# Performance work log

Hardware: AMD Instinct MI355X
Metric: run time of the kernel (lower is better)

The kernel has to match this reference:

```python
import jax, jax.numpy as jnp
import numpy as np

N = 120000
G = 64  # voxel grid side
HID = 128
INP = 320
CIN = HID + INP  # 448
K = 27


def _build_neighbor_map(rng):
    # unique occupied voxel cells
    cells = rng.choice(G ** 3, size=N, replace=False)
    xs = cells // (G * G)
    ys = (cells // G) % G
    zs = cells % G
    order = np.argsort(cells)
    sk = cells[order]
    offs = np.array([(dx, dy, dz) for dx in (-1, 0, 1) for dy in (-1, 0, 1) for dz in (-1, 0, 1)], dtype=np.int64)
    nx = xs[:, None] + offs[None, :, 0]
    ny = ys[:, None] + offs[None, :, 1]
    nz = zs[:, None] + offs[None, :, 2]
    valid = (nx >= 0) & (nx < G) & (ny >= 0) & (ny < G) & (nz >= 0) & (nz < G)
    nkey = (nx * G + ny) * G + nz
    pos = np.clip(np.searchsorted(sk, nkey), 0, N - 1)
    found = valid & (sk[pos] == nkey)
    return np.where(found, order[pos], -1).astype(np.int32)  # (N, 27)


def setup_inputs() -> dict:
    key = jax.random.key(0)
    ks = jax.random.split(key, 12)
    rng = np.random.default_rng(0)
    nbr = jnp.asarray(_build_neighbor_map(rng))
    s_conv = 1.0 / np.sqrt(K * CIN)
    s_lin = 1.0 / np.sqrt(CIN)
    return {
        "h": jax.random.normal(ks[0], (N, HID), jnp.float32),
        "x": jax.random.normal(ks[1], (N, INP), jnp.float32),
        "nbr": nbr,
        "Wz": jax.random.normal(ks[2], (K, CIN, HID), jnp.float32) * s_conv,
        "Wz_pt": jax.random.normal(ks[3], (CIN, HID), jnp.float32) * s_lin,
        "bz": jnp.zeros((HID,), jnp.float32),
        "Wr": jax.random.normal(ks[4], (K, CIN, HID), jnp.float32) * s_conv,
        "Wr_pt": jax.random.normal(ks[5], (CIN, HID), jnp.float32) * s_lin,
        "br": jnp.zeros((HID,), jnp.float32),
        "Wq": jax.random.normal(ks[6], (K, CIN, HID), jnp.float32) * s_conv,
        "Wq_pt": jax.random.normal(ks[7], (CIN, HID), jnp.float32) * s_lin,
        "bq": jnp.zeros((HID,), jnp.float32),
    }


def _sconv3d(F, nbr, W, W_pt, b_pt):
    # sparse 3x3x3 conv (gather + matmul accumulate over 27 offsets, no conv bias)
    # followed by voxel_to_point (identity here) + point_transforms linear.
    mask = (nbr >= 0)
    idx = jnp.where(mask, nbr, 0)
    out = F @ W_pt + b_pt  # point transform branch
    for k in range(K):  # fixed small kernel-offset loop
        g = F[idx[:, k]] * mask[:, k:k + 1].astype(F.dtype)  # (N, CIN)
        out = out + g @ W[k]
    return out


def reference(h, x, nbr, Wz, Wz_pt, bz, Wr, Wr_pt, br, Wq, Wq_pt, bq):
    hx = jnp.concatenate([h, x], axis=1)  # (N, 448)
    z = jax.nn.sigmoid(_sconv3d(hx, nbr, Wz, Wz_pt, bz))
    r = jax.nn.sigmoid(_sconv3d(hx, nbr, Wr, Wr_pt, br))
    rx = jnp.concatenate([r * h, x], axis=1)
    q = jnp.tanh(_sconv3d(rx, nbr, Wq, Wq_pt, bq))
    return (1.0 - z) * h + z * q
```

## Files before the change

kernel.cpp:

```cpp
#include <hip/hip_runtime.h>

#define NPTS   120000
#define NOFF   28
#define CHUNKS 7

typedef __bf16 bf16;
typedef __bf16 bf16x8 __attribute__((ext_vector_type(8)));
typedef float  f32x4  __attribute__((ext_vector_type(4)));

__global__ void wprep1(const float* __restrict__ Wz, const float* __restrict__ Wzp,
                       const float* __restrict__ Wr, const float* __restrict__ Wrp,
                       bf16* __restrict__ WB1)
{
    int bid  = blockIdx.x;
    int koff = bid / 56;
    int rem  = bid % 56;
    int ch   = rem / 8;
    int kseg = rem % 8;
    int n    = threadIdx.x;
    int cinb = ch * 64 + kseg * 8;
    bf16x8 v;
    if (n < 128) {
        int col = n;
        #pragma unroll
        for (int j = 0; j < 8; ++j) {
            int cin = cinb + j;
            float w = (koff < 27) ? Wz[((long)koff * 448 + cin) * 128 + col]
                                  : Wzp[(long)cin * 128 + col];
            v[j] = (bf16)w;
        }
    } else {
        int col = n - 128;
        #pragma unroll
        for (int j = 0; j < 8; ++j) {
            int cin = cinb + j;
            float w = (koff < 27) ? Wr[((long)koff * 448 + cin) * 128 + col]
                                  : Wrp[(long)cin * 128 + col];
            v[j] = (bf16)w;
        }
    }
    *(bf16x8*)(WB1 + ((long)bid * 256 + n) * 8) = v;
}

__global__ void wprep2(const float* __restrict__ Wq, const float* __restrict__ Wqp,
                       bf16* __restrict__ WB2)
{
    int bid  = blockIdx.x;
    int koff = bid / 56;
    int rem  = bid % 56;
    int ch   = rem / 8;
    int kseg = rem % 8;
    int n    = threadIdx.x;
    int cinb = ch * 64 + kseg * 8;
    bf16x8 v;
    #pragma unroll
    for (int j = 0; j < 8; ++j) {
        int cin = cinb + j;
        float w = (koff < 27) ? Wq[((long)koff * 448 + cin) * 128 + n]
                              : Wqp[(long)cin * 128 + n];
        v[j] = (bf16)w;
    }
    *(bf16x8*)(WB2 + ((long)bid * 128 + n) * 8) = v;
}

__global__ void fprep(const float* __restrict__ h, const float* __restrict__ x,
                      bf16* __restrict__ F1)
{
    long g = (long)blockIdx.x * blockDim.x + threadIdx.x;
    if (g >= (long)NPTS * 56) return;
    int p = (int)(g / 56);
    int c = (int)(g % 56) * 8;
    const float* src = (c < 128) ? h + (long)p * 128 + c
                                 : x + (long)p * 320 + (c - 128);
    float4 a = ((const float4*)src)[0];
    float4 b = ((const float4*)src)[1];
    bf16x8 v;
    v[0] = (bf16)a.x; v[1] = (bf16)a.y; v[2] = (bf16)a.z; v[3] = (bf16)a.w;
    v[4] = (bf16)b.x; v[5] = (bf16)b.y; v[6] = (bf16)b.z; v[7] = (bf16)b.w;
    *(bf16x8*)(F1 + (long)p * 448 + c) = v;
}

template<int MROWS, int NCOLS, int GATE>
__global__ __launch_bounds__(512)
void gconv(const bf16* __restrict__ F, const int* __restrict__ nbr,
           const bf16* __restrict__ WB, const float* __restrict__ b0,
           const float* __restrict__ b1, const float* __restrict__ hbuf,
           float* __restrict__ zbuf, bf16* __restrict__ f2,
           float* __restrict__ out, const bf16* __restrict__ zrow)
{
    constexpr int THREADS = 512;
    constexpr int MW = MROWS / 64;
    constexpr int AP = 8 * MROWS / THREADS;
    constexpr int BP = 8 * NCOLS / THREADS;

    __shared__ __align__(16) bf16 lA[8 * MROWS * 8];
    __shared__ __align__(16) bf16 lB[8 * NCOLS * 8];
    __shared__ int lidx[MROWS];

    const int t    = threadIdx.x;
    const int lane = t & 63;
    const int w    = t >> 6;
    const int m0   = (w % MW) * 64;
    const int n0   = (w / MW) * 64;
    const int base = blockIdx.x * MROWS;
    const int ar   = t % MROWS;
    const int aks0 = t / MROWS;

    f32x4 acc[4][4];
    #pragma unroll
    for (int i = 0; i < 4; ++i)
        #pragma unroll
        for (int j = 0; j < 4; ++j)
            acc[i][j] = {0.f, 0.f, 0.f, 0.f};

    const bf16x8* lAv = (const bf16x8*)lA;
    const bf16x8* lBv = (const bf16x8*)lB;

    for (int koff = 0; koff < NOFF; ++koff) {
        __syncthreads();
        if (t < MROWS) {
            int p = base + t;
            int idx = -1;
            if (p < NPTS) idx = (koff == 27) ? p : nbr[(long)p * 27 + koff];
            lidx[t] = idx;
        }
        __syncthreads();
        const int myidx = lidx[ar];
        const bf16* row1 = (myidx >= 0) ? (F + (long)myidx * 448) : zrow;
        const bf16* row2 = row1;
        if constexpr (GATE == 2)
            row2 = (myidx >= 0) ? (f2 + (long)myidx * 128) : zrow;

        for (int ch = 0; ch < CHUNKS; ++ch) {
            const bf16* asrc = (GATE == 2 && ch < 2) ? (row2 + ch * 64)
                                                     : (row1 + ch * 64);
            #pragma unroll
            for (int p = 0; p < AP; ++p) {
                int kseg = aks0 + p * (THREADS / MROWS);
                __builtin_amdgcn_global_load_lds(
                    (void*)(asrc + kseg * 8),
                    (void*)(lA + ((long)t + (long)p * THREADS) * 8),
                    16, 0, 0);
            }
            const bf16* bsrc = WB + (long)(koff * CHUNKS + ch) * (NCOLS * 64);
            #pragma unroll
            for (int p = 0; p < BP; ++p) {
                __builtin_amdgcn_global_load_lds(
                    (void*)(bsrc + ((long)t + (long)p * THREADS) * 8),
                    (void*)(lB + ((long)t + (long)p * THREADS) * 8),
                    16, 0, 0);
            }
            __syncthreads();
            #pragma unroll
            for (int kk = 0; kk < 2; ++kk) {
                const int aseg = kk * 4 + (lane >> 4);
                bf16x8 af[4], bfr[4];
                #pragma unroll
                for (int mi = 0; mi < 4; ++mi)
                    af[mi] = lAv[aseg * MROWS + m0 + mi * 16 + (lane & 15)];
                #pragma unroll
                for (int ni = 0; ni < 4; ++ni)
                    bfr[ni] = lBv[aseg * NCOLS + n0 + ni * 16 + (lane & 15)];
                #pragma unroll
                for (int mi = 0; mi < 4; ++mi)
                    #pragma unroll
                    for (int ni = 0; ni < 4; ++ni)
                        acc[mi][ni] = __builtin_amdgcn_mfma_f32_16x16x32_bf16(
                            af[mi], bfr[ni], acc[mi][ni], 0, 0, 0);
            }
            __syncthreads();
        }
    }

    const int quad = lane >> 4;
    const int lc   = lane & 15;
    #pragma unroll
    for (int mi = 0; mi < 4; ++mi) {
        int rb = m0 + mi * 16 + quad * 4;
        #pragma unroll
        for (int ni = 0; ni < 4; ++ni) {
            int c = n0 + ni * 16 + lc;
            f32x4 v = acc[mi][ni];
            #pragma unroll
            for (int rg = 0; rg < 4; ++rg) {
                int p = base + rb + rg;
                if (p < NPTS) {
                    float pre = v[rg];
                    if constexpr (GATE == 1) {
                        if (c < 128) {
                            float z = 1.f / (1.f + __expf(-(pre + b0[c])));
                            zbuf[(long)p * 128 + c] = z;
                        } else {
                            int cc = c - 128;
                            float r = 1.f / (1.f + __expf(-(pre + b1[cc])));
                            f2[(long)p * 128 + cc] = (bf16)(r * hbuf[(long)p * 128 + cc]);
                        }
                    } else {
                        float q  = tanhf(pre + b0[c]);
                        float z  = zbuf[(long)p * 128 + c];
                        float hv = hbuf[(long)p * 128 + c];
                        out[(long)p * 128 + c] = (1.f - z) * hv + z * q;
                    }
                }
            }
        }
    }
}

extern "C" void kernel_launch(void* const* d_in, const int* in_sizes, int n_in,
                              void* d_out, int out_size, void* d_ws, size_t ws_size,
                              hipStream_t stream)
{
    const float* h   = (const float*)d_in[0];
    const float* x   = (const float*)d_in[1];
    const int*   nbr = (const int*)d_in[2];
    const float* Wz  = (const float*)d_in[3];
    const float* Wzp = (const float*)d_in[4];
    const float* bz  = (const float*)d_in[5];
    const float* Wr  = (const float*)d_in[6];
    const float* Wrp = (const float*)d_in[7];
    const float* br  = (const float*)d_in[8];
    const float* Wq  = (const float*)d_in[9];
    const float* Wqp = (const float*)d_in[10];
    const float* bq  = (const float*)d_in[11];
    float* out = (float*)d_out;

    char* ws = (char*)d_ws;
    bf16* WB1 = (bf16*)ws;  ws += (size_t)1568 * 256 * 8 * 2;
    bf16* WB2 = (bf16*)ws;  ws += (size_t)1568 * 128 * 8 * 2;
    bf16* F1  = (bf16*)ws;  ws += (size_t)NPTS * 448 * 2;
    bf16* F2  = (bf16*)ws;  ws += (size_t)NPTS * 128 * 2;
    bf16* zrow = (bf16*)ws; ws += 1024;
    float* zbuf = out;

    hipMemsetAsync(zrow, 0, 1024, stream);
    wprep1<<<1568, 256, 0, stream>>>(Wz, Wzp, Wr, Wrp, WB1);
    wprep2<<<1568, 128, 0, stream>>>(Wq, Wqp, WB2);
    long groups = (long)NPTS * 56;
    fprep<<<(int)((groups + 255) / 256), 256, 0, stream>>>(h, x, F1);

    gconv<128, 256, 1><<<(NPTS + 127) / 128, 512, 0, stream>>>(
        F1, nbr, WB1, bz, br, h, zbuf, F2, nullptr, zrow);
    gconv<256, 128, 2><<<(NPTS + 255) / 256, 512, 0, stream>>>(
        F1, nbr, WB2, bq, nullptr, h, zbuf, F2, out, zrow);
}
```

Before: 1.537 ms.

## Multi-stage LDS pipeline for gather-conv with prefetched neighbor indices

Replaces the single-buffered load/sync/compute loop with a 2- or 3-stage circular LDS buffer. The next gathered rows and weight chunks are issued asynchronously while MFMAs run on the current stage, using explicit vmcnt waits and raw barriers. All 28 offset indices for the block are preloaded into LDS up front, which removes the two per-offset barriers, and setprio raises priority around the MFMA burst. The extra stages increase LDS use and may reduce occupancy.

```diff
diff --git a/kernel.cpp b/kernel.cpp
--- a/kernel.cpp
+++ b/kernel.cpp
@@ -3,6 +3,7 @@
 #define NPTS   120000
 #define NOFF   28
 #define CHUNKS 7
+#define NSTEP  (NOFF * CHUNKS)
 
 typedef __bf16 bf16;
 typedef __bf16 bf16x8 __attribute__((ext_vector_type(8)));
@@ -89,13 +90,17 @@
            float* __restrict__ out, const bf16* __restrict__ zrow)
 {
     constexpr int THREADS = 512;
-    constexpr int MW = MROWS / 64;
-    constexpr int AP = 8 * MROWS / THREADS;
-    constexpr int BP = 8 * NCOLS / THREADS;
-
-    __shared__ __align__(16) bf16 lA[8 * MROWS * 8];
-    __shared__ __align__(16) bf16 lB[8 * NCOLS * 8];
-    __shared__ int lidx[MROWS];
+    constexpr int MW  = MROWS / 64;
+    constexpr int AP  = 8 * MROWS / THREADS;
+    constexpr int BP  = 8 * NCOLS / THREADS;
+    constexpr int STG = (GATE == 1) ? 3 : 2;
+    constexpr int ASZ = 8 * MROWS * 8;
+    constexpr int BSZ = 8 * NCOLS * 8;
+    constexpr int LPB = AP + BP;
+
+    __shared__ __align__(16) bf16 lA[STG * ASZ];
+    __shared__ __align__(16) bf16 lB[STG * BSZ];
+    __shared__ int lidx[NOFF * MROWS];
 
     const int t    = threadIdx.x;
     const int lane = t & 63;
@@ -106,6 +111,15 @@
     const int ar   = t % MROWS;
     const int aks0 = t / MROWS;
 
+    for (int i = t; i < NOFF * MROWS; i += THREADS) {
+        int k = i / MROWS, r = i - k * MROWS;
+        int p = base + r;
+        int idx = -1;
+        if (p < NPTS) idx = (k == 27) ? p : nbr[(long)p * 27 + k];
+        lidx[i] = idx;
+    }
+    __syncthreads();
+
     f32x4 acc[4][4];
     #pragma unroll
     for (int i = 0; i < 4; ++i)
@@ -113,63 +127,77 @@
         for (int j = 0; j < 4; ++j)
             acc[i][j] = {0.f, 0.f, 0.f, 0.f};
 
-    const bf16x8* lAv = (const bf16x8*)lA;
-    const bf16x8* lBv = (const bf16x8*)lB;
-
-    for (int koff = 0; koff < NOFF; ++koff) {
-        __syncthreads();
-        if (t < MROWS) {
-            int p = base + t;
-            int idx = -1;
-            if (p < NPTS) idx = (koff == 27) ? p : nbr[(long)p * 27 + koff];
-            lidx[t] = idx;
-        }
-        __syncthreads();
-        const int myidx = lidx[ar];
-        const bf16* row1 = (myidx >= 0) ? (F + (long)myidx * 448) : zrow;
-        const bf16* row2 = row1;
-        if constexpr (GATE == 2)
-            row2 = (myidx >= 0) ? (f2 + (long)myidx * 128) : zrow;
-
-        for (int ch = 0; ch < CHUNKS; ++ch) {
-            const bf16* asrc = (GATE == 2 && ch < 2) ? (row2 + ch * 64)
-                                                     : (row1 + ch * 64);
-            #pragma unroll
-            for (int p = 0; p < AP; ++p) {
-                int kseg = aks0 + p * (THREADS / MROWS);
-                __builtin_amdgcn_global_load_lds(
-                    (void*)(asrc + kseg * 8),
-                    (void*)(lA + ((long)t + (long)p * THREADS) * 8),
-                    16, 0, 0);
-            }
-            const bf16* bsrc = WB + (long)(koff * CHUNKS + ch) * (NCOLS * 64);
-            #pragma unroll
-            for (int p = 0; p < BP; ++p) {
-                __builtin_amdgcn_global_load_lds(
-                    (void*)(bsrc + ((long)t + (long)p * THREADS) * 8),
-                    (void*)(lB + ((long)t + (long)p * THREADS) * 8),
-                    16, 0, 0);
-            }
-            __syncthreads();
-            #pragma unroll
-            for (int kk = 0; kk < 2; ++kk) {
-                const int aseg = kk * 4 + (lane >> 4);
-                bf16x8 af[4], bfr[4];
-                #pragma unroll
-                for (int mi = 0; mi < 4; ++mi)
-                    af[mi] = lAv[aseg * MROWS + m0 + mi * 16 + (lane & 15)];
+    auto stage = [&](int s) {
+        const int koff = s / CHUNKS;
+        const int ch   = s - koff * CHUNKS;
+        const int bsl  = s % STG;
+        const int idx  = lidx[koff * MROWS + ar];
+        const bf16* asrc;
+        if constexpr (GATE == 2) {
+            asrc = (idx < 0) ? zrow
+                 : (ch < 2)  ? f2 + (long)idx * 128 + ch * 64
+                             : F  + (long)idx * 448 + ch * 64;
+        } else {
+            asrc = (idx < 0) ? zrow : F + (long)idx * 448 + ch * 64;
+        }
+        bf16* la = lA + bsl * ASZ;
+        #pragma unroll
+        for (int p = 0; p < AP; ++p) {
+            int kseg = aks0 + p * (THREADS / MROWS);
+            __builtin_amdgcn_global_load_lds(
+                (void*)(asrc + kseg * 8),
+                (void*)(la + ((long)t + (long)p * THREADS) * 8), 16, 0, 0);
+        }
+        const bf16* bsrc = WB + (long)s * (NCOLS * 64);
+        bf16* lb = lB + bsl * BSZ;
+        #pragma unroll
+        for (int p = 0; p < BP; ++p) {
+            __builtin_amdgcn_global_load_lds(
+                (void*)(bsrc + ((long)t + (long)p * THREADS) * 8),
+                (void*)(lb + ((long)t + (long)p * THREADS) * 8), 16, 0, 0);
+        }
+    };
+
+    #pragma unroll
+    for (int s = 0; s < STG - 1; ++s) stage(s);
+
+    for (int s = 0; s < NSTEP; ++s) {
+        if (s + STG - 1 < NSTEP) stage(s + STG - 1);
+
+        if constexpr (STG == 3) {
+            if (s + 2 < NSTEP)      asm volatile("s_waitcnt vmcnt(%0)" :: "i"(2 * LPB) : "memory");
+            else if (s + 1 < NSTEP) asm volatile("s_waitcnt vmcnt(%0)" :: "i"(LPB) : "memory");
+            else                    asm volatile("s_waitcnt vmcnt(0)" ::: "memory");
+        } else {
+            if (s + 1 < NSTEP)      asm volatile("s_waitcnt vmcnt(%0)" :: "i"(LPB) : "memory");
+            else                    asm volatile("s_waitcnt vmcnt(0)" ::: "memory");
+        }
+        __builtin_amdgcn_s_barrier();
+        __builtin_amdgcn_sched_barrier(0);
+
+        const bf16x8* lAv = (const bf16x8*)(lA + (s % STG) * ASZ);
+        const bf16x8* lBv = (const bf16x8*)(lB + (s % STG) * BSZ);
+        #pragma unroll
+        for (int kk = 0; kk < 2; ++kk) {
+            const int aseg = kk * 4 + (lane >> 4);
+            bf16x8 af[4], bfr[4];
+            #pragma unroll
+            for (int mi = 0; mi < 4; ++mi)
+                af[mi] = lAv[aseg * MROWS + m0 + mi * 16 + (lane & 15)];
+            #pragma unroll
+            for (int ni = 0; ni < 4; ++ni)
+                bfr[ni] = lBv[aseg * NCOLS + n0 + ni * 16 + (lane & 15)];
+            __builtin_amdgcn_s_setprio(1);
+            #pragma unroll
+            for (int mi = 0; mi < 4; ++mi)
                 #pragma unroll
                 for (int ni = 0; ni < 4; ++ni)
-                    bfr[ni] = lBv[aseg * NCOLS + n0 + ni * 16 + (lane & 15)];
-                #pragma unroll
-                for (int mi = 0; mi < 4; ++mi)
-                    #pragma unroll
-                    for (int ni = 0; ni < 4; ++ni)
-                        acc[mi][ni] = __builtin_amdgcn_mfma_f32_16x16x32_bf16(
-                            af[mi], bfr[ni], acc[mi][ni], 0, 0, 0);
-            }
-            __syncthreads();
-        }
+                    acc[mi][ni] = __builtin_amdgcn_mfma_f32_16x16x32_bf16(
+                        af[mi], bfr[ni], acc[mi][ni], 0, 0, 0);
+            __builtin_amdgcn_s_setprio(0);
+        }
+        __builtin_amdgcn_sched_barrier(0);
+        __builtin_amdgcn_s_barrier();
     }
 
     const int quad = lane >> 4;
```

Measured after the change: 2.269 ms. 1.48x slower.

## Add double-buffered 256x256 gate conv kernel with async global-to-LDS prefetch

Applied to the files above, without the earlier changes.

Replaces the first gated sparse-conv launch (z and r gates) with a new kernel that uses a larger 256-row by 256-column tile and double-buffered LDS. It prefetches the next step's gathered activation rows and weight slice directly into LDS with global_load_lds while MFMAs run on the current buffer. All 28 offsets' neighbor indices are preloaded once per block. The aim is to hide gather latency and halve weight reloads per row. The cost is heavier LDS use, a fine-grained barrier and waitcnt schedule, and fewer blocks for 120k points.

```diff
diff --git a/kernel.cpp b/kernel.cpp
--- a/kernel.cpp
+++ b/kernel.cpp
@@ -3,6 +3,7 @@
 #define NPTS   120000
 #define NOFF   28
 #define CHUNKS 7
+#define NSTEP  (NOFF * CHUNKS)
 
 typedef __bf16 bf16;
 typedef __bf16 bf16x8 __attribute__((ext_vector_type(8)));
@@ -78,6 +79,193 @@
     v[0] = (bf16)a.x; v[1] = (bf16)a.y; v[2] = (bf16)a.z; v[3] = (bf16)a.w;
     v[4] = (bf16)b.x; v[5] = (bf16)b.y; v[6] = (bf16)b.z; v[7] = (bf16)b.w;
     *(bf16x8*)(F1 + (long)p * 448 + c) = v;
+}
+
+__global__ __launch_bounds__(512, 2)
+void gconv1p(const bf16* __restrict__ F, const int* __restrict__ nbr,
+             const bf16* __restrict__ WB, const float* __restrict__ b0,
+             const float* __restrict__ b1, const float* __restrict__ hbuf,
+             float* __restrict__ zbuf, bf16* __restrict__ f2,
+             const bf16* __restrict__ zrow)
+{
+    constexpr int BM = 256, BN = 256;
+    constexpr int ASZ = 8 * BM * 8;
+    constexpr int BSZ = 8 * BN * 8;
+
+    __shared__ __align__(16) bf16 lA[2 * ASZ];
+    __shared__ __align__(16) bf16 lB[2 * BSZ];
+    __shared__ int lidx[NOFF * BM];
+
+    const int t    = threadIdx.x;
+    const int lane = t & 63;
+    const int w    = t >> 6;
+    const int m0   = (w & 1) * 128;
+    const int n0   = (w >> 1) * 64;
+    const int base = blockIdx.x * BM;
+    const int ar   = t & 255;
+    const int aks0 = t >> 8;
+
+    for (int i = t; i < NOFF * BM; i += 512) {
+        int k = i >> 8, r = i & 255;
+        int p = base + r;
+        int idx = -1;
+        if (p < NPTS) idx = (k == 27) ? p : nbr[(long)p * 27 + k];
+        lidx[i] = idx;
+    }
+    __syncthreads();
+
+    f32x4 acc[8][4];
+    #pragma unroll
+    for (int i = 0; i < 8; ++i)
+        #pragma unroll
+        for (int j = 0; j < 4; ++j)
+            acc[i][j] = {0.f, 0.f, 0.f, 0.f};
+
+    auto issueA = [&](int idx, int ch, int slot, int p) {
+        const bf16* asrc = (idx < 0) ? zrow : F + (long)idx * 448 + ch * 64;
+        const int kseg = aks0 + 2 * p;
+        __builtin_amdgcn_global_load_lds(
+            (void*)(asrc + kseg * 8),
+            (void*)(lA + slot * ASZ + (((kseg << 8) | ar) * 8)), 16, 0, 0);
+    };
+    auto issueB = [&](int s, int slot, int p) {
+        const bf16* bsrc = WB + (long)s * (BN * 64);
+        const int e = t + p * 512;
+        __builtin_amdgcn_global_load_lds(
+            (void*)(bsrc + (long)e * 8),
+            (void*)(lB + slot * BSZ + (long)e * 8), 16, 0, 0);
+    };
+
+    {
+        const int idx0 = lidx[ar];
+        #pragma unroll
+        for (int p = 0; p < 4; ++p) issueA(idx0, 0, 0, p);
+        #pragma unroll
+        for (int p = 0; p < 4; ++p) issueB(0, 0, p);
+        asm volatile("s_waitcnt vmcnt(0)" ::: "memory");
+        __syncthreads();
+    }
+
+    const bf16x8* lAv = (const bf16x8*)lA;
+    const bf16x8* lBv = (const bf16x8*)lB;
+    const int lc = lane & 15;
+    const int q4 = lane >> 4;
+
+    for (int s = 0; s < NSTEP; ++s) {
+        const int slot  = s & 1;
+        const int nslot = slot ^ 1;
+        const bool pf   = (s + 1 < NSTEP);
+        const int koff1 = (s + 1) / CHUNKS;
+        const int ch1   = (s + 1) - koff1 * CHUNKS;
+        const int nidx  = pf ? lidx[(koff1 << 8) | ar] : 0;
+
+        const int av = slot * (ASZ / 8);
+        const int bv = slot * (BSZ / 8);
+        const int a0 = q4;
+        const int a1 = 4 + q4;
+
+        bf16x8 af[4], bfr[4];
+
+        #pragma unroll
+        for (int m = 0; m < 4; ++m) af[m]  = lAv[av + a0 * 256 + m0 + m * 16 + lc];
+        #pragma unroll
+        for (int n = 0; n < 4; ++n) bfr[n] = lBv[bv + a0 * 256 + n0 + n * 16 + lc];
+        if (pf) { issueA(nidx, ch1, nslot, 0); issueB(s + 1, nslot, 0); }
+        __builtin_amdgcn_sched_barrier(0);
+        __builtin_amdgcn_s_barrier();
+        asm volatile("s_waitcnt lgkmcnt(0)" ::: "memory");
+        __builtin_amdgcn_sched_barrier(0);
+        __builtin_amdgcn_s_setprio(1);
+        #pragma unroll
+        for (int m = 0; m < 4; ++m)
+            #pragma unroll
+            for (int n = 0; n < 4; ++n)
+                acc[m][n] = __builtin_amdgcn_mfma_f32_16x16x32_bf16(af[m], bfr[n], acc[m][n], 0, 0, 0);
+        __builtin_amdgcn_s_setprio(0);
+        __builtin_amdgcn_sched_barrier(0);
+        __builtin_amdgcn_s_barrier();
+
+        #pragma unroll
+        for (int m = 0; m < 4; ++m) af[m] = lAv[av + a0 * 256 + m0 + 64 + m * 16 + lc];
+        if (pf) { issueA(nidx, ch1, nslot, 1); issueB(s + 1, nslot, 1); }
+        __builtin_amdgcn_sched_barrier(0);
+        __builtin_amdgcn_s_barrier();
+        asm volatile("s_waitcnt lgkmcnt(0)" ::: "memory");
+        __builtin_amdgcn_sched_barrier(0);
+        __builtin_amdgcn_s_setprio(1);
+        #pragma unroll
+        for (int m = 0; m < 4; ++m)
+            #pragma unroll
+            for (int n = 0; n < 4; ++n)
+                acc[4 + m][n] = __builtin_amdgcn_mfma_f32_16x16x32_bf16(af[m], bfr[n], acc[4 + m][n], 0, 0, 0);
+        __builtin_amdgcn_s_setprio(0);
+        __builtin_amdgcn_sched_barrier(0);
+        if (pf) asm volatile("s_waitcnt vmcnt(4)" ::: "memory");
+        else    asm volatile("s_waitcnt vmcnt(0)" ::: "memory");
+        __builtin_amdgcn_s_barrier();
+
+        #pragma unroll
+        for (int m = 0; m < 4; ++m) af[m]  = lAv[av + a1 * 256 + m0 + m * 16 + lc];
+        #pragma unroll
+        for (int n = 0; n < 4; ++n) bfr[n] = lBv[bv + a1 * 256 + n0 + n * 16 + lc];
+        if (pf) { issueA(nidx, ch1, nslot, 2); issueB(s + 1, nslot, 2); }
+        __builtin_amdgcn_sched_barrier(0);
+        __builtin_amdgcn_s_barrier();
+        asm volatile("s_waitcnt lgkmcnt(0)" ::: "memory");
+        __builtin_amdgcn_sched_barrier(0);
+        __builtin_amdgcn_s_setprio(1);
+        #pragma unroll
+        for (int m = 0; m < 4; ++m)
+            #pragma unroll
+            for (int n = 0; n < 4; ++n)
+                acc[m][n] = __builtin_amdgcn_mfma_f32_16x16x32_bf16(af[m], bfr[n], acc[m][n], 0, 0, 0);
+        __builtin_amdgcn_s_setprio(0);
+        __builtin_amdgcn_sched_barrier(0);
+        __builtin_amdgcn_s_barrier();
+
+        #pragma unroll
+        for (int m = 0; m < 4; ++m) af[m] = lAv[av + a1 * 256 + m0 + 64 + m * 16 + lc];
+        if (pf) { issueA(nidx, ch1, nslot, 3); issueB(s + 1, nslot, 3); }
+        __builtin_amdgcn_sched_barrier(0);
+        __builtin_amdgcn_s_barrier();
+        asm volatile("s_waitcnt lgkmcnt(0)" ::: "memory");
+        __builtin_amdgcn_sched_barrier(0);
+        __builtin_amdgcn_s_setprio(1);
+        #pragma unroll
+        for (int m = 0; m < 4; ++m)
+            #pragma unroll
+            for (int n = 0; n < 4; ++n)
+                acc[4 + m][n] = __builtin_amdgcn_mfma_f32_16x16x32_bf16(af[m], bfr[n], acc[4 + m][n], 0, 0, 0);
+        __builtin_amdgcn_s_setprio(0);
+        __builtin_amdgcn_sched_barrier(0);
+        if (pf) asm volatile("s_waitcnt vmcnt(4)" ::: "memory");
+        __builtin_amdgcn_s_barrier();
+    }
+
+    #pragma unroll
+    for (int mi = 0; mi < 8; ++mi) {
+        int rb = m0 + mi * 16 + q4 * 4;
+        #pragma unroll
+        for (int ni = 0; ni < 4; ++ni) {
+            int c = n0 + ni * 16 + lc;
+            f32x4 v = acc[mi][ni];
+            #pragma unroll
+            for (int rg = 0; rg < 4; ++rg) {
+                int p = base + rb + rg;
+                if (p < NPTS) {
+                    float pre = v[rg];
+                    if (c < 128) {
+                        float z = 1.f / (1.f + __expf(-(pre + b0[c])));
+                        zbuf[(long)p * 128 + c] = z;
+                    } else {
+                        int cc = c - 128;
+                        float r = 1.f / (1.f + __expf(-(pre + b1[cc])));
+                        f2[(long)p * 128 + cc] = (bf16)(r * hbuf[(long)p * 128 + cc]);
+                    }
+                }
+            }
+        }
+    }
 }
 
 template<int MROWS, int NCOLS, int GATE>
@@ -239,8 +427,8 @@
     long groups = (long)NPTS * 56;
     fprep<<<(int)((groups + 255) / 256), 256, 0, stream>>>(h, x, F1);
 
-    gconv<128, 256, 1><<<(NPTS + 127) / 128, 512, 0, stream>>>(
-        F1, nbr, WB1, bz, br, h, zbuf, F2, nullptr, zrow);
+    gconv1p<<<(NPTS + 255) / 256, 512, 0, stream>>>(
+        F1, nbr, WB1, bz, br, h, zbuf, F2, zrow);
     gconv<256, 128, 2><<<(NPTS + 255) / 256, 512, 0, stream>>>(
         F1, nbr, WB2, bq, nullptr, h, zbuf, F2, out, zrow);
 }
```

New measurement: 1.735 ms. 12.9% more time.
